# Kernel optimization log

Measured on AMD Instinct MI355X. Metric: run time of the kernel, lower is better.

Reference implementation:

```python
import jax, jax.numpy as jnp
import numpy as np

B, D, H, HD, P, O, K = 256, 1024, 8, 128, 2048, 1024, 4
HID = H * HD
EPS = 1e-5


def setup_inputs() -> dict:
    key = jax.random.key(0)
    ks = jax.random.split(key, 16)

    def w(k, shape, fan_in):
        return jax.random.normal(k, shape, jnp.float32) / np.sqrt(fan_in).astype(np.float32)

    return dict(
        seq=jax.random.normal(ks[0], (B, D), jnp.float32),
        c_tm1=jnp.zeros((B, H, HD, HD), jnp.float32),
        n_tm1=jnp.ones((B, H, HD), jnp.float32),
        m_tm1=jnp.zeros((B, H), jnp.float32),
        ln_g=jnp.ones((D,), jnp.float32), ln_b=jnp.zeros((D,), jnp.float32),
        gn_g=jnp.ones((HID,), jnp.float32), gn_b=jnp.zeros((HID,), jnp.float32),
        W_upl=w(ks[1], (P, D), D), b_upl=jnp.zeros((P,), jnp.float32),
        W_upr=w(ks[2], (HID, D), D), b_upr=jnp.zeros((HID,), jnp.float32),
        W_down=w(ks[3], (D, HID), HID), b_down=jnp.zeros((D,), jnp.float32),
        W_last=w(ks[4], (O, D), D), b_last=jnp.zeros((O,), jnp.float32),
        conv_w=w(ks[5], (K,), K), conv_b=jnp.zeros((), jnp.float32),
        W_skip=w(ks[6], (HID, P), P),
        W_i=w(ks[7], (H, P), P), b_i=jnp.zeros((H,), jnp.float32),
        W_f=w(ks[8], (H, P), P), b_f=jnp.zeros((H,), jnp.float32),
        W_o=w(ks[9], (HID, P), P), b_o=jnp.zeros((HID,), jnp.float32),
        W_q=w(ks[10], (HID, P), P), b_q=jnp.zeros((HID,), jnp.float32),
        W_k=w(ks[11], (HID, P), P), b_k=jnp.zeros((HID,), jnp.float32),
        W_v=w(ks[12], (HID, P), P), b_v=jnp.zeros((HID,), jnp.float32),
    )


def reference(seq, c_tm1, n_tm1, m_tm1, ln_g, ln_b, gn_g, gn_b,
              W_upl, b_upl, W_upr, b_upr, W_down, b_down, W_last, b_last,
              conv_w, conv_b, W_skip, W_i, b_i, W_f, b_f, W_o, b_o,
              W_q, b_q, W_k, b_k, W_v, b_v):
    b = seq.shape[0]
    h, hd = c_tm1.shape[1], c_tm1.shape[2]

    # input LayerNorm
    mu = jnp.mean(seq, -1, keepdims=True)
    var = jnp.var(seq, -1, keepdims=True)
    x_n = (seq - mu) * jax.lax.rsqrt(var + EPS) * ln_g + ln_b

    x_t = x_n @ W_upl.T + b_upl            # [b, P]
    r_t = x_n @ W_upr.T + b_upr            # [b, HID]

    # causal conv over the feature axis (in=out=1 channel), left pad K-1
    k_sz = conv_w.shape[0]
    p = x_t.shape[1]
    xp = jnp.pad(x_t, ((0, 0), (k_sz - 1, 0)))
    x_c = conv_b + sum(conv_w[j] * xp[:, j:j + p] for j in range(k_sz))
    x_c = jax.nn.silu(x_c)                 # [b, P]

    q_t = (x_c @ W_q.T + b_q).reshape(b, h, hd)
    k_t = ((x_c @ W_k.T + b_k) / np.sqrt(hd).astype(np.float32)).reshape(b, h, hd)
    v_t = (x_t @ W_v.T + b_v).reshape(b, h, hd)

    i_t = x_c @ W_i.T + b_i                # [b, h]
    f_t = x_c @ W_f.T + b_f                # [b, h]
    o_t = jax.nn.sigmoid(x_t @ W_o.T + b_o)  # [b, HID]

    # stabilized exponential gating
    m_t = jnp.maximum(f_t + m_tm1, i_t)
    i_g = jnp.exp(i_t - m_t)
    f_g = jnp.exp(f_t - m_t + m_tm1)

    # matrix-memory covariance update
    c_t = f_g[:, :, None, None] * c_tm1 + i_g[:, :, None, None] * jnp.einsum('bhd,bhp->bhdp', v_t, k_t)
    n_t = f_g[:, :, None] * n_tm1 + i_g[:, :, None] * k_t

    num = jnp.einsum('bhdp,bhp->bhd', c_t, q_t)
    den = jnp.maximum(jnp.einsum('bhd,bhd->bh', n_t, q_t), 1.0)
    h_t = o_t * (num / den[:, :, None]).reshape(b, h * hd)

    # GroupNorm(head_num groups) over hidden
    hg = h_t.reshape(b, h, hd)
    gmu = jnp.mean(hg, -1, keepdims=True)
    gvar = jnp.var(hg, -1, keepdims=True)
    hn = ((hg - gmu) * jax.lax.rsqrt(gvar + EPS)).reshape(b, h * hd) * gn_g + gn_b

    out = hn + x_c @ W_skip.T              # 1x1 conv skip == matmul
    out = out * jax.nn.silu(r_t)
    out = out @ W_down.T + b_down
    final = (out + x_n) @ W_last.T + b_last
    return final, c_t, n_t, m_t
```

## Files before the change

kernel.cpp:

```cpp
#include <hip/hip_runtime.h>
#include <cstdint>
#include <cstddef>

#define LN_EPS 1e-5f

typedef float  f32x4  __attribute__((ext_vector_type(4)));
typedef __bf16 bf16x8 __attribute__((ext_vector_type(8)));
typedef unsigned short u16x4 __attribute__((ext_vector_type(4)));

__device__ __forceinline__ float block_sum(float v, volatile float* red) {
#pragma unroll
  for (int o = 32; o > 0; o >>= 1) v += __shfl_down(v, o, 64);
  const int lane = threadIdx.x & 63, w = threadIdx.x >> 6;
  __syncthreads();
  if (lane == 0) red[w] = v;
  __syncthreads();
  return red[0] + red[1] + red[2] + red[3];
}

__global__ __launch_bounds__(256)
void k_ln(const float* __restrict__ seq, const float* __restrict__ g,
          const float* __restrict__ b, float* __restrict__ xn) {
  __shared__ float red[8];
  const int row = blockIdx.x, t = threadIdx.x;
  const f32x4 x = ((const f32x4*)(seq + (size_t)row * 1024))[t];
  float s  = x[0] + x[1] + x[2] + x[3];
  float s2 = x[0]*x[0] + x[1]*x[1] + x[2]*x[2] + x[3]*x[3];
#pragma unroll
  for (int o = 32; o > 0; o >>= 1) { s += __shfl_down(s, o, 64); s2 += __shfl_down(s2, o, 64); }
  const int lane = t & 63, w = t >> 6;
  if (lane == 0) { red[w] = s; red[4 + w] = s2; }
  __syncthreads();
  s  = red[0] + red[1] + red[2] + red[3];
  s2 = red[4] + red[5] + red[6] + red[7];
  const float mu  = s * (1.f / 1024.f);
  const float inv = rsqrtf(s2 * (1.f / 1024.f) - mu * mu + LN_EPS);
  const f32x4 gg = ((const f32x4*)g)[t];
  const f32x4 bb = ((const f32x4*)b)[t];
  f32x4 y;
#pragma unroll
  for (int i = 0; i < 4; ++i) y[i] = (x[i] - mu) * inv * gg[i] + bb[i];
  ((f32x4*)(xn + (size_t)row * 1024))[t] = y;
}

__global__ __launch_bounds__(256)
void k_conv(const float* __restrict__ xt, const float* __restrict__ cw,
            const float* __restrict__ cb, float* __restrict__ xc) {
  __shared__ float s[2048];
  const int row = blockIdx.x, t = threadIdx.x;
  const f32x4* src = (const f32x4*)(xt + (size_t)row * 2048);
  ((f32x4*)s)[t] = src[t];
  ((f32x4*)s)[t + 256] = src[t + 256];
  const float w0 = cw[0], w1 = cw[1], w2 = cw[2], w3 = cw[3], b = cb[0];
  __syncthreads();
  float out[8];
  const int c0 = t * 8;
#pragma unroll
  for (int j = 0; j < 8; ++j) {
    const int c = c0 + j;
    float a = b + w3 * s[c];
    if (c >= 1) a += w2 * s[c - 1];
    if (c >= 2) a += w1 * s[c - 2];
    if (c >= 3) a += w0 * s[c - 3];
    a = a / (1.f + __expf(-a));
    out[j] = a;
  }
  f32x4* dst = (f32x4*)(xc + (size_t)row * 2048 + c0);
  f32x4 v0 = {out[0], out[1], out[2], out[3]};
  f32x4 v1 = {out[4], out[5], out[6], out[7]};
  dst[0] = v0; dst[1] = v1;
}

__global__ __launch_bounds__(256)
void k_if(const float* __restrict__ xc, const float* __restrict__ Wi,
          const float* __restrict__ bi, const float* __restrict__ Wf,
          const float* __restrict__ bfp, const float* __restrict__ m_tm1,
          float* __restrict__ m_out, float* __restrict__ ig, float* __restrict__ fg) {
  __shared__ float sx[2048];
  __shared__ float so[16];
  const int row = blockIdx.x, t = threadIdx.x;
  const f32x4* src = (const f32x4*)(xc + (size_t)row * 2048);
  ((f32x4*)sx)[t] = src[t];
  ((f32x4*)sx)[t + 256] = src[t + 256];
  __syncthreads();
  const int w = t >> 6, lane = t & 63;
  float p[4];
#pragma unroll
  for (int i = 0; i < 4; ++i) {
    const int o = w * 4 + i;
    const float* wr = (o < 8) ? (Wi + (size_t)o * 2048) : (Wf + (size_t)(o - 8) * 2048);
    float acc = 0.f;
#pragma unroll
    for (int j = 0; j < 8; ++j) {
      const f32x4 xv = ((const f32x4*)sx)[j * 64 + lane];
      const f32x4 wv = ((const f32x4*)wr)[j * 64 + lane];
      acc += xv[0]*wv[0] + xv[1]*wv[1] + xv[2]*wv[2] + xv[3]*wv[3];
    }
    p[i] = acc;
  }
#pragma unroll
  for (int i = 0; i < 4; ++i) {
#pragma unroll
    for (int o = 32; o > 0; o >>= 1) p[i] += __shfl_xor(p[i], o, 64);
  }
  if (lane == 0) {
#pragma unroll
    for (int i = 0; i < 4; ++i) so[w * 4 + i] = p[i];
  }
  __syncthreads();
  if (t < 8) {
    const float it = so[t] + bi[t];
    const float ft = so[t + 8] + bfp[t];
    const float mp = m_tm1[row * 8 + t];
    const float m = fmaxf(ft + mp, it);
    m_out[row * 8 + t] = m;
    ig[row * 8 + t] = __expf(it - m);
    fg[row * 8 + t] = __expf(ft - m + mp);
  }
}

__global__ __launch_bounds__(256)
void k_rec_stream(const float* __restrict__ c_tm1, const float* __restrict__ kb,
                  const float* __restrict__ qb, const float* __restrict__ vb,
                  const float* __restrict__ ig, const float* __restrict__ fg,
                  float* __restrict__ c_out, float* __restrict__ numG) {
  const int blk = blockIdx.x;
  const int bh = blk >> 2;
  const int rg = blk & 3;
  const int t = threadIdx.x;
  const int w = t >> 6, lane = t & 63;
  const int c4 = lane & 31;
  const int half = lane >> 5;
  const int b = bh >> 3, h = bh & 7;
  const size_t vecbase = (size_t)b * 1024 + h * 128;
  const float fgv = fg[bh], igv = ig[bh];
  const f32x4 k4 = ((const f32x4*)(kb + vecbase))[c4];
  const f32x4 q4 = ((const f32x4*)(qb + vecbase))[c4];
  const int row0 = rg * 32 + w * 8;
  const f32x4* C0 = (const f32x4*)(c_tm1 + (size_t)bh * 16384);
  f32x4* Ct = (f32x4*)(c_out + (size_t)bh * 16384);
  f32x4 c0s[4]; float vrow[4];
#pragma unroll
  for (int j = 0; j < 4; ++j) {
    const int r = row0 + 2 * j + half;
    c0s[j] = C0[r * 32 + c4];
    vrow[j] = vb[vecbase + r];
  }
  float pd[4];
#pragma unroll
  for (int j = 0; j < 4; ++j) {
    const int r = row0 + 2 * j + half;
    const float iv = igv * vrow[j];
    f32x4 ct = fgv * c0s[j] + iv * k4;
    __builtin_nontemporal_store(ct, Ct + r * 32 + c4);
    pd[j] = ct[0] * q4[0] + ct[1] * q4[1] + ct[2] * q4[2] + ct[3] * q4[3];
  }
#pragma unroll
  for (int j = 0; j < 4; ++j) {
    float p = pd[j];
    p += __shfl_xor(p, 1, 64); p += __shfl_xor(p, 2, 64); p += __shfl_xor(p, 4, 64);
    p += __shfl_xor(p, 8, 64); p += __shfl_xor(p, 16, 64);
    if (c4 == 0) numG[(size_t)bh * 128 + row0 + 2 * j + half] = p;
  }
}

__device__ __forceinline__ float bsum128(float v, volatile float* red) {
#pragma unroll
  for (int o = 32; o > 0; o >>= 1) v += __shfl_xor(v, o, 64);
  const int w = threadIdx.x >> 6;
  __syncthreads();
  if ((threadIdx.x & 63) == 0) red[w] = v;
  __syncthreads();
  return red[0] + red[1];
}

__global__ __launch_bounds__(128)
void k_rec_fin(const float* __restrict__ n_tm1, const float* __restrict__ kb,
               const float* __restrict__ qb, const float* __restrict__ ot,
               const float* __restrict__ ig, const float* __restrict__ fg,
               const float* __restrict__ numG,
               const float* __restrict__ gn_g, const float* __restrict__ gn_b,
               const float* __restrict__ skipb, const float* __restrict__ sr,
               float* __restrict__ n_out, float* __restrict__ uf) {
  __shared__ float red[2];
  const int bh = blockIdx.x, t = threadIdx.x;
  const int b = bh >> 3, h = bh & 7;
  const size_t base = (size_t)b * 1024 + h * 128;
  const float fgv = fg[bh], igv = ig[bh];
  const float ntd = fgv * n_tm1[(size_t)bh * 128 + t] + igv * kb[base + t];
  n_out[(size_t)bh * 128 + t] = ntd;
  const float den = fmaxf(bsum128(ntd * qb[base + t], red), 1.f);
  const float o = 1.f / (1.f + __expf(-ot[base + t]));
  const float hv = o * numG[(size_t)bh * 128 + t] / den;
  const float mu  = bsum128(hv, red) * (1.f / 128.f);
  const float var = bsum128(hv * hv, red) * (1.f / 128.f) - mu * mu;
  const int hid = h * 128 + t;
  const float hn = (hv - mu) * rsqrtf(var + LN_EPS) * gn_g[hid] + gn_b[hid];
  uf[base + t] = (hn + skipb[base + t]) * sr[base + t];
}

struct GemmSeg {
  const float* A; const float* W; const float* bias; float* out;
  const float* add; int ldOut; int colOfs; int epi; float scale;
};
struct GemmArgs { GemmSeg seg[5]; };

__global__ __launch_bounds__(256)
void k_gemm(int K, GemmArgs ga) {
  __shared__ __align__(16) char lds[2][32768];
  const int tid = threadIdx.x;
  const int lane = tid & 63;
  const int wid = tid >> 6;
  const int wm = wid >> 1;
  const int wn = wid & 1;
  const int segId = blockIdx.x >> 4;
  const int n0 = (blockIdx.x & 15) * 64;
  const int m0 = blockIdx.y * 64;
  const GemmSeg sg = ga.seg[segId];

  const int lrow = tid >> 4;
  const int col4 = tid & 15;

  f32x4 acc[2][2] = {};

  const float* Abase = sg.A + (size_t)m0 * K;
  const float* Wbase = sg.W + (size_t)n0 * K;
  const int NT = K >> 6;

  f32x4 va[4], vw[4], va2[4], vw2[4];
#pragma unroll
  for (int p = 0; p < 4; ++p) {
    const int r = p * 16 + lrow;
    va[p] = *(const f32x4*)(Abase + (size_t)r * K + col4 * 4);
    vw[p] = *(const f32x4*)(Wbase + (size_t)r * K + col4 * 4);
  }

  for (int kt = 0; kt < NT; ++kt) {
    {
      char* lb = lds[kt & 1];
      const int byte = ((((col4 >> 1) ^ (lrow & 7)) << 4) | ((col4 & 1) << 3));
#pragma unroll
      for (int p = 0; p < 4; ++p) {
        const int r = p * 16 + lrow;
        u16x4 ah, al, wh, wl;
#pragma unroll
        for (int i = 0; i < 4; ++i) {
          const unsigned ab = __float_as_uint(va[p][i]);
          const float fh = __uint_as_float(ab & 0xFFFF0000u);
          ah[i] = (unsigned short)(ab >> 16);
          al[i] = (unsigned short)(__float_as_uint(va[p][i] - fh) >> 16);
          const unsigned wb2 = __float_as_uint(vw[p][i]);
          const float wfh = __uint_as_float(wb2 & 0xFFFF0000u);
          wh[i] = (unsigned short)(wb2 >> 16);
          wl[i] = (unsigned short)(__float_as_uint(vw[p][i] - wfh) >> 16);
        }
        *(u16x4*)(lb + r * 128 + byte) = ah;
        *(u16x4*)(lb + 8192 + r * 128 + byte) = al;
        *(u16x4*)(lb + 16384 + r * 128 + byte) = wh;
        *(u16x4*)(lb + 24576 + r * 128 + byte) = wl;
      }
    }
    if (kt + 1 < NT) {
      const int ko = (kt + 1) * 64;
#pragma unroll
      for (int p = 0; p < 4; ++p) {
        const int r = p * 16 + lrow;
        va2[p] = *(const f32x4*)(Abase + (size_t)r * K + ko + col4 * 4);
        vw2[p] = *(const f32x4*)(Wbase + (size_t)r * K + ko + col4 * 4);
      }
    }
    __syncthreads();
    {
      const char* lb = lds[kt & 1];
      const int rA = wm * 32 + (lane & 15);
      const int rB = wn * 32 + (lane & 15);
      const int kg = lane >> 4;
      const int swz = lane & 7;
#pragma unroll
      for (int kk = 0; kk < 2; ++kk) {
        const int so = ((kk * 4 + kg) ^ swz) << 4;
        const char* pa0 = lb + rA * 128 + so;
        const char* pa1 = lb + (rA + 16) * 128 + so;
        const char* pb0 = lb + 16384 + rB * 128 + so;
        const char* pb1 = lb + 16384 + (rB + 16) * 128 + so;
        const bf16x8 ah0 = *(const bf16x8*)(pa0);
        const bf16x8 al0 = *(const bf16x8*)(pa0 + 8192);
        const bf16x8 ah1 = *(const bf16x8*)(pa1);
        const bf16x8 al1 = *(const bf16x8*)(pa1 + 8192);
        const bf16x8 bh0 = *(const bf16x8*)(pb0);
        const bf16x8 bl0 = *(const bf16x8*)(pb0 + 8192);
        const bf16x8 bh1 = *(const bf16x8*)(pb1);
        const bf16x8 bl1 = *(const bf16x8*)(pb1 + 8192);
        acc[0][0] = __builtin_amdgcn_mfma_f32_16x16x32_bf16(ah0, bh0, acc[0][0], 0, 0, 0);
        acc[0][1] = __builtin_amdgcn_mfma_f32_16x16x32_bf16(ah0, bh1, acc[0][1], 0, 0, 0);
        acc[1][0] = __builtin_amdgcn_mfma_f32_16x16x32_bf16(ah1, bh0, acc[1][0], 0, 0, 0);
        acc[1][1] = __builtin_amdgcn_mfma_f32_16x16x32_bf16(ah1, bh1, acc[1][1], 0, 0, 0);
        acc[0][0] = __builtin_amdgcn_mfma_f32_16x16x32_bf16(ah0, bl0, acc[0][0], 0, 0, 0);
        acc[0][1] = __builtin_amdgcn_mfma_f32_16x16x32_bf16(ah0, bl1, acc[0][1], 0, 0, 0);
        acc[1][0] = __builtin_amdgcn_mfma_f32_16x16x32_bf16(ah1, bl0, acc[1][0], 0, 0, 0);
        acc[1][1] = __builtin_amdgcn_mfma_f32_16x16x32_bf16(ah1, bl1, acc[1][1], 0, 0, 0);
        acc[0][0] = __builtin_amdgcn_mfma_f32_16x16x32_bf16(al0, bh0, acc[0][0], 0, 0, 0);
        acc[0][1] = __builtin_amdgcn_mfma_f32_16x16x32_bf16(al0, bh1, acc[0][1], 0, 0, 0);
        acc[1][0] = __builtin_amdgcn_mfma_f32_16x16x32_bf16(al1, bh0, acc[1][0], 0, 0, 0);
        acc[1][1] = __builtin_amdgcn_mfma_f32_16x16x32_bf16(al1, bh1, acc[1][1], 0, 0, 0);
      }
    }
#pragma unroll
    for (int p = 0; p < 4; ++p) { va[p] = va2[p]; vw[p] = vw2[p]; }
    __syncthreads();
  }

  const int rowb = m0 + wm * 32 + (lane >> 4) * 4;
  const int colb = n0 + wn * 32 + (lane & 15);
#pragma unroll
  for (int mf = 0; mf < 2; ++mf) {
#pragma unroll
    for (int nf = 0; nf < 2; ++nf) {
      const int col = colb + nf * 16;
      const float bv = sg.bias ? sg.bias[col] : 0.f;
#pragma unroll
      for (int i = 0; i < 4; ++i) {
        const int row = rowb + mf * 16 + i;
        float v = acc[mf][nf][i] + bv;
        if (sg.epi == 1)      v = v / (1.f + __expf(-v));
        else if (sg.epi == 3) v *= sg.scale;
        else if (sg.epi == 4) v += sg.add[(size_t)row * 1024 + col];
        sg.out[(size_t)row * sg.ldOut + sg.colOfs + col] = v;
      }
    }
  }
}

extern "C" void kernel_launch(void* const* d_in, const int* in_sizes, int n_in,
                              void* d_out, int out_size, void* d_ws, size_t ws_size,
                              hipStream_t stream) {
  (void)in_sizes; (void)n_in; (void)out_size; (void)ws_size;
  const float* seq    = (const float*)d_in[0];
  const float* c_tm1  = (const float*)d_in[1];
  const float* n_tm1  = (const float*)d_in[2];
  const float* m_tm1  = (const float*)d_in[3];
  const float* ln_g   = (const float*)d_in[4];
  const float* ln_b   = (const float*)d_in[5];
  const float* gn_g   = (const float*)d_in[6];
  const float* gn_b   = (const float*)d_in[7];
  const float* W_upl  = (const float*)d_in[8];
  const float* b_upl  = (const float*)d_in[9];
  const float* W_upr  = (const float*)d_in[10];
  const float* b_upr  = (const float*)d_in[11];
  const float* W_down = (const float*)d_in[12];
  const float* b_down = (const float*)d_in[13];
  const float* W_last = (const float*)d_in[14];
  const float* b_last = (const float*)d_in[15];
  const float* conv_w = (const float*)d_in[16];
  const float* conv_b = (const float*)d_in[17];
  const float* W_skip = (const float*)d_in[18];
  const float* W_i    = (const float*)d_in[19];
  const float* b_i    = (const float*)d_in[20];
  const float* W_f    = (const float*)d_in[21];
  const float* b_f    = (const float*)d_in[22];
  const float* W_o    = (const float*)d_in[23];
  const float* b_o    = (const float*)d_in[24];
  const float* W_q    = (const float*)d_in[25];
  const float* b_q    = (const float*)d_in[26];
  const float* W_k    = (const float*)d_in[27];
  const float* b_k    = (const float*)d_in[28];
  const float* W_v    = (const float*)d_in[29];
  const float* b_v    = (const float*)d_in[30];

  float* out_final = (float*)d_out;
  float* out_c = out_final + (size_t)256 * 1024;
  float* out_n = out_c + (size_t)256 * 8 * 128 * 128;
  float* out_m = out_n + (size_t)256 * 8 * 128;

  char* ws = (char*)d_ws;
  size_t off = 0;
  auto alloc = [&](size_t bytes) -> void* {
    void* p = ws + off; off += (bytes + 255) & ~(size_t)255; return p;
  };
  float* x_n   = (float*)alloc((size_t)256 * 1024 * 4);
  float* x_t   = (float*)alloc((size_t)256 * 2048 * 4);
  float* sr    = (float*)alloc((size_t)256 * 1024 * 4);
  float* x_c   = (float*)alloc((size_t)256 * 2048 * 4);
  float* qb    = (float*)alloc((size_t)256 * 1024 * 4);
  float* kb    = (float*)alloc((size_t)256 * 1024 * 4);
  float* vb    = (float*)alloc((size_t)256 * 1024 * 4);
  float* otb   = (float*)alloc((size_t)256 * 1024 * 4);
  float* skipb = (float*)alloc((size_t)256 * 1024 * 4);
  float* igb   = (float*)alloc((size_t)2048 * 4);
  float* fgb   = (float*)alloc((size_t)2048 * 4);
  float* u_f   = (float*)alloc((size_t)256 * 1024 * 4);
  float* t_f   = (float*)alloc((size_t)256 * 1024 * 4);
  float* numG  = (float*)alloc((size_t)2048 * 128 * 4);

  k_ln<<<256, 256, 0, stream>>>(seq, ln_g, ln_b, x_n);

  GemmArgs gA = {};
  gA.seg[0] = {x_n, W_upl, b_upl, x_t, nullptr, 2048, 0, 0, 0.f};
  gA.seg[1] = {x_n, W_upl + (size_t)1024 * 1024, b_upl + 1024, x_t, nullptr, 2048, 1024, 0, 0.f};
  gA.seg[2] = {x_n, W_upr, b_upr, sr, nullptr, 1024, 0, 1, 0.f};
  k_gemm<<<dim3(48, 4), 256, 0, stream>>>(1024, gA);

  k_conv<<<256, 256, 0, stream>>>(x_t, conv_w, conv_b, x_c);

  k_if<<<256, 256, 0, stream>>>(x_c, W_i, b_i, W_f, b_f, m_tm1, out_m, igb, fgb);

  GemmArgs gBC = {};
  gBC.seg[0] = {x_c, W_q, b_q, qb, nullptr, 1024, 0, 0, 0.f};
  gBC.seg[1] = {x_c, W_k, b_k, kb, nullptr, 1024, 0, 3, 0.08838834764831845f};
  gBC.seg[2] = {x_c, W_skip, nullptr, skipb, nullptr, 1024, 0, 0, 0.f};
  gBC.seg[3] = {x_t, W_v, b_v, vb, nullptr, 1024, 0, 0, 0.f};
  gBC.seg[4] = {x_t, W_o, b_o, otb, nullptr, 1024, 0, 0, 0.f};
  k_gemm<<<dim3(80, 4), 256, 0, stream>>>(2048, gBC);

  k_rec_stream<<<8192, 256, 0, stream>>>(c_tm1, kb, qb, vb, igb, fgb, out_c, numG);

  k_rec_fin<<<2048, 128, 0, stream>>>(n_tm1, kb, qb, otb, igb, fgb, numG,
                                      gn_g, gn_b, skipb, sr, out_n, u_f);

  GemmArgs gD = {};
  gD.seg[0] = {u_f, W_down, b_down, t_f, x_n, 1024, 0, 4, 0.f};
  k_gemm<<<dim3(16, 4), 256, 0, stream>>>(1024, gD);

  GemmArgs gE = {};
  gE.seg[0] = {t_f, W_last, b_last, out_final, nullptr, 1024, 0, 0, 0.f};
  k_gemm<<<dim3(16, 4), 256, 0, stream>>>(1024, gE);
}
```

Measured before the change: 163.4 us.

## Fuse conv with i/f gating kernel and widen recurrence-stream blocks

Merges the causal-conv kernel and the input/forget gate projection kernel into one launch, so the conv output is handed to the gate dot products through shared memory and not re-read from global memory. The matrix-memory update kernel now has each block cover 64 rows instead of 32, which halves the grid and doubles the loads in flight per thread. Its c_t stores also change from nontemporal to normal stores. The trade-offs are more shared memory per block in the fused kernel, more registers in the stream kernel, and possible cache pollution from the 32MB c_t output.

New measurement: 172.5 us. +5.5%, slower.

```diff
diff --git a/kernel.cpp b/kernel.cpp
--- a/kernel.cpp
+++ b/kernel.cpp
@@ -7,16 +7,6 @@
 typedef float  f32x4  __attribute__((ext_vector_type(4)));
 typedef __bf16 bf16x8 __attribute__((ext_vector_type(8)));
 typedef unsigned short u16x4 __attribute__((ext_vector_type(4)));
-
-__device__ __forceinline__ float block_sum(float v, volatile float* red) {
-#pragma unroll
-  for (int o = 32; o > 0; o >>= 1) v += __shfl_down(v, o, 64);
-  const int lane = threadIdx.x & 63, w = threadIdx.x >> 6;
-  __syncthreads();
-  if (lane == 0) red[w] = v;
-  __syncthreads();
-  return red[0] + red[1] + red[2] + red[3];
-}
 
 __global__ __launch_bounds__(256)
 void k_ln(const float* __restrict__ seq, const float* __restrict__ g,
@@ -44,9 +34,15 @@
 }
 
 __global__ __launch_bounds__(256)
-void k_conv(const float* __restrict__ xt, const float* __restrict__ cw,
-            const float* __restrict__ cb, float* __restrict__ xc) {
+void k_conv_if(const float* __restrict__ xt, const float* __restrict__ cw,
+               const float* __restrict__ cb, float* __restrict__ xc,
+               const float* __restrict__ Wi, const float* __restrict__ bi,
+               const float* __restrict__ Wf, const float* __restrict__ bfp,
+               const float* __restrict__ m_tm1, float* __restrict__ m_out,
+               float* __restrict__ ig, float* __restrict__ fg) {
   __shared__ float s[2048];
+  __shared__ float sx[2048];
+  __shared__ float so[16];
   const int row = blockIdx.x, t = threadIdx.x;
   const f32x4* src = (const f32x4*)(xt + (size_t)row * 2048);
   ((f32x4*)s)[t] = src[t];
@@ -65,23 +61,12 @@
     a = a / (1.f + __expf(-a));
     out[j] = a;
   }
-  f32x4* dst = (f32x4*)(xc + (size_t)row * 2048 + c0);
   f32x4 v0 = {out[0], out[1], out[2], out[3]};
   f32x4 v1 = {out[4], out[5], out[6], out[7]};
+  f32x4* dst = (f32x4*)(xc + (size_t)row * 2048 + c0);
   dst[0] = v0; dst[1] = v1;
-}
-
-__global__ __launch_bounds__(256)
-void k_if(const float* __restrict__ xc, const float* __restrict__ Wi,
-          const float* __restrict__ bi, const float* __restrict__ Wf,
-          const float* __restrict__ bfp, const float* __restrict__ m_tm1,
-          float* __restrict__ m_out, float* __restrict__ ig, float* __restrict__ fg) {
-  __shared__ float sx[2048];
-  __shared__ float so[16];
-  const int row = blockIdx.x, t = threadIdx.x;
-  const f32x4* src = (const f32x4*)(xc + (size_t)row * 2048);
-  ((f32x4*)sx)[t] = src[t];
-  ((f32x4*)sx)[t + 256] = src[t + 256];
+  ((f32x4*)sx)[t * 2] = v0;
+  ((f32x4*)sx)[t * 2 + 1] = v1;
   __syncthreads();
   const int w = t >> 6, lane = t & 63;
   float p[4];
@@ -125,8 +110,8 @@
                   const float* __restrict__ ig, const float* __restrict__ fg,
                   float* __restrict__ c_out, float* __restrict__ numG) {
   const int blk = blockIdx.x;
-  const int bh = blk >> 2;
-  const int rg = blk & 3;
+  const int bh = blk >> 1;
+  const int rg = blk & 1;
   const int t = threadIdx.x;
   const int w = t >> 6, lane = t & 63;
   const int c4 = lane & 31;
@@ -136,27 +121,27 @@
   const float fgv = fg[bh], igv = ig[bh];
   const f32x4 k4 = ((const f32x4*)(kb + vecbase))[c4];
   const f32x4 q4 = ((const f32x4*)(qb + vecbase))[c4];
-  const int row0 = rg * 32 + w * 8;
+  const int row0 = rg * 64 + w * 16;
   const f32x4* C0 = (const f32x4*)(c_tm1 + (size_t)bh * 16384);
   f32x4* Ct = (f32x4*)(c_out + (size_t)bh * 16384);
-  f32x4 c0s[4]; float vrow[4];
-#pragma unroll
-  for (int j = 0; j < 4; ++j) {
+  f32x4 c0s[8]; float vrow[8];
+#pragma unroll
+  for (int j = 0; j < 8; ++j) {
     const int r = row0 + 2 * j + half;
     c0s[j] = C0[r * 32 + c4];
     vrow[j] = vb[vecbase + r];
   }
-  float pd[4];
-#pragma unroll
-  for (int j = 0; j < 4; ++j) {
+  float pd[8];
+#pragma unroll
+  for (int j = 0; j < 8; ++j) {
     const int r = row0 + 2 * j + half;
     const float iv = igv * vrow[j];
     f32x4 ct = fgv * c0s[j] + iv * k4;
-    __builtin_nontemporal_store(ct, Ct + r * 32 + c4);
+    Ct[r * 32 + c4] = ct;
     pd[j] = ct[0] * q4[0] + ct[1] * q4[1] + ct[2] * q4[2] + ct[3] * q4[3];
   }
 #pragma unroll
-  for (int j = 0; j < 4; ++j) {
+  for (int j = 0; j < 8; ++j) {
     float p = pd[j];
     p += __shfl_xor(p, 1, 64); p += __shfl_xor(p, 2, 64); p += __shfl_xor(p, 4, 64);
     p += __shfl_xor(p, 8, 64); p += __shfl_xor(p, 16, 64);
@@ -400,9 +385,8 @@
   gA.seg[2] = {x_n, W_upr, b_upr, sr, nullptr, 1024, 0, 1, 0.f};
   k_gemm<<<dim3(48, 4), 256, 0, stream>>>(1024, gA);
 
-  k_conv<<<256, 256, 0, stream>>>(x_t, conv_w, conv_b, x_c);
-
-  k_if<<<256, 256, 0, stream>>>(x_c, W_i, b_i, W_f, b_f, m_tm1, out_m, igb, fgb);
+  k_conv_if<<<256, 256, 0, stream>>>(x_t, conv_w, conv_b, x_c,
+                                     W_i, b_i, W_f, b_f, m_tm1, out_m, igb, fgb);
 
   GemmArgs gBC = {};
   gBC.seg[0] = {x_c, W_q, b_q, qb, nullptr, 1024, 0, 0, 0.f};
@@ -412,7 +396,7 @@
   gBC.seg[4] = {x_t, W_o, b_o, otb, nullptr, 1024, 0, 0, 0.f};
   k_gemm<<<dim3(80, 4), 256, 0, stream>>>(2048, gBC);
 
-  k_rec_stream<<<8192, 256, 0, stream>>>(c_tm1, kb, qb, vb, igb, fgb, out_c, numG);
+  k_rec_stream<<<4096, 256, 0, stream>>>(c_tm1, kb, qb, vb, igb, fgb, out_c, numG);
 
   k_rec_fin<<<2048, 128, 0, stream>>>(n_tm1, kb, qb, otb, igb, fgb, numG,
                                       gn_g, gn_b, skipb, sr, out_n, u_f);
```
